# Performance work log

Measured on AMD Instinct MI355X. Metric: run time of the kernel, lower is better.

The kernel has to match this reference:

```python
import jax, jax.numpy as jnp
import numpy as np

T, B, D, H = 512, 512, 512, 512

def setup_inputs() -> dict:
    key = jax.random.key(0)
    k_in, k_wih, k_whh, k_bih, k_bhh = jax.random.split(key, 5)
    s = 1.0 / np.sqrt(H)  # torch RNNCell init scale
    return {
        "inputs": jax.random.normal(k_in, (T, B, D), dtype=jnp.float32),
        "W_ih": jax.random.uniform(k_wih, (H, D), jnp.float32, -s, s),
        "W_hh": jax.random.uniform(k_whh, (H, H), jnp.float32, -s, s),
        "b_ih": jax.random.uniform(k_bih, (H,), jnp.float32, -s, s),
        "b_hh": jax.random.uniform(k_bhh, (H,), jnp.float32, -s, s),
        "hidden_size": H,
    }

def reference(inputs, W_ih, W_hh, b_ih, b_hh, hidden_size):
    # h_{t+1} = tanh(x_t @ W_ih^T + b_ih + h_t @ W_hh^T + b_hh)
    # Original inits hidden with inputs.shape[0] rows (quirk: requires T == B).
    h0 = jnp.zeros((inputs.shape[0], hidden_size), dtype=inputs.dtype)
    # Precompute the input projection for all steps in one big GEMM;
    # the recurrence itself must remain sequential.
    xp = jnp.einsum("tbd,hd->tbh", inputs, W_ih) + b_ih + b_hh  # [T, B, H]

    def step(h, xp_t):
        h = jnp.tanh(xp_t + h @ W_hh.T)
        return h, None

    h_final, _ = jax.lax.scan(step, h0, xp)
    return h_final
```

## Files before the change

### kernel.cpp

```cpp
#include <hip/hip_runtime.h>
#include <stdint.h>

#define TSTEPS 512
#define NB 512
#define ND 512
#define NH 512
#define SENT 0xFFFFFFFFFFFFFFFFull

typedef _Float16 half8 __attribute__((ext_vector_type(8)));
typedef float float4v __attribute__((ext_vector_type(4)));
typedef unsigned long long u64;

__device__ __forceinline__ float fast_tanh(float x) {
  float e = __expf(2.0f * x);
  return 1.0f - 2.0f * __builtin_amdgcn_rcpf(e + 1.0f);
}

#define AL(p)    __hip_atomic_load((p), __ATOMIC_RELAXED, __HIP_MEMORY_SCOPE_AGENT)
#define AS(p, v) __hip_atomic_store((p), (v), __ATOMIC_RELAXED, __HIP_MEMORY_SCOPE_AGENT)

#define LDSBAR()                                                               \
  do {                                                                         \
    asm volatile("s_waitcnt lgkmcnt(0)" ::: "memory");                         \
    __builtin_amdgcn_s_barrier();                                              \
  } while (0)

#define PREFETCH_X(XP, TN)                                                     \
  do {                                                                         \
    const float* xrow_ = x + ((size_t)(TN) * NB + myrow) * ND + kbase + quad * 8; \
    _Pragma("unroll")                                                          \
    for (int kk = 0; kk < 4; ++kk) {                                           \
      XP[kk][0] = *(const float4v*)(xrow_ + kk * 32);                          \
      XP[kk][1] = *(const float4v*)(xrow_ + kk * 32 + 4);                      \
    }                                                                          \
  } while (0)

__global__ void __launch_bounds__(256, 1)
rnn_persistent(const float* __restrict__ x,
               const float* __restrict__ Wih,
               const float* __restrict__ Whh,
               const float* __restrict__ bih,
               const float* __restrict__ bhh,
               float* __restrict__ out,
               _Float16* __restrict__ hbuf)
{
  __shared__ __attribute__((aligned(16))) float red[2][4][16][68];

  const int bid  = blockIdx.x;
  const int grp  = bid & 31;
  const int cwg  = bid >> 5;
  const int wave = threadIdx.x >> 6;
  const int lane = threadIdx.x & 63;
  const int m    = lane & 15;
  const int quad = lane >> 4;
  const int tid  = threadIdx.x;

  const int R     = grp * 16;
  const int C0    = cwg * 64;
  const int kbase = wave * 128;

  half8 wih_f[4][4];
  half8 whh_f[4][4];
  #pragma unroll
  for (int tile = 0; tile < 4; ++tile) {
    const int n = C0 + tile * 16 + m;
    const float* wr_ih = Wih + (size_t)n * ND;
    const float* wr_hh = Whh + (size_t)n * NH;
    #pragma unroll
    for (int kk = 0; kk < 4; ++kk) {
      const int k0 = kbase + kk * 32 + quad * 8;
      half8 a, b;
      #pragma unroll
      for (int j = 0; j < 8; ++j) {
        a[j] = (_Float16)wr_ih[k0 + j];
        b[j] = (_Float16)wr_hh[k0 + j];
      }
      wih_f[kk][tile] = a;
      whh_f[kk][tile] = b;
    }
  }

  const int prow = tid >> 4;
  const int pcol = (tid & 15) * 4;
  float4v bias4;
  #pragma unroll
  for (int j = 0; j < 4; ++j)
    bias4[j] = bih[C0 + pcol + j] + bhh[C0 + pcol + j];

  const int myrow = R + m;
  const int orow  = quad * 4;

  float4v xvA[4][2], xvB[4][2];
  {
    const float* xrow0 = x + (size_t)myrow * ND + kbase + quad * 8;
    #pragma unroll
    for (int kk = 0; kk < 4; ++kk) {
      xvA[kk][0] = *(const float4v*)(xrow0 + kk * 32);
      xvA[kk][1] = *(const float4v*)(xrow0 + kk * 32 + 4);
    }
  }

#define STEP(T, PAR, XU, XP)                                                   \
  {                                                                            \
    const int t_ = (T);                                                        \
        \
    if (t_ >= 2) {                                                             \
      u64* cl = (u64*)(hbuf + (size_t)((t_ + 2) & 3) * NB * NH +               \
                       (size_t)(R + prow) * NH + C0 + pcol);                   \
      AS(cl, SENT);                                                            \
    }                                                                          \
    float4v acc[4];                                                            \
    _Pragma("unroll")                                                          \
    for (int tile = 0; tile < 4; ++tile) acc[tile] = (float4v){0.f,0.f,0.f,0.f};\
                                         \
    _Pragma("unroll")                                                          \
    for (int kk = 0; kk < 4; ++kk) {                                           \
      half8 a;                                                                 \
      _Pragma("unroll")                                                        \
      for (int j = 0; j < 4; ++j) {                                            \
        a[j]     = (_Float16)XU[kk][0][j];                                     \
        a[j + 4] = (_Float16)XU[kk][1][j];                                     \
      }                                                                        \
      _Pragma("unroll")                                                        \
      for (int tile = 0; tile < 4; ++tile)                                     \
        acc[tile] = __builtin_amdgcn_mfma_f32_16x16x32_f16(a, wih_f[kk][tile], acc[tile], 0, 0, 0); \
    }                                                                          \
    if (t_ > 0) {                                                              \
      const int tn_ = (t_ + 1 < TSTEPS) ? (t_ + 1) : t_;                       \
      const _Float16* hb = hbuf + (size_t)(t_ & 3) * NB * NH;                  \
      const u64* hrow = (const u64*)(hb + (size_t)myrow * NH + kbase + quad * 8); \
                                           \
      u64 w0 = AL(hrow + 0), w1 = AL(hrow + 1);                                \
      u64 w2 = AL(hrow + 8), w3 = AL(hrow + 9);                                \
      u64 w4 = AL(hrow + 16), w5 = AL(hrow + 17);                              \
      u64 w6 = AL(hrow + 24), w7 = AL(hrow + 25);                              \
      PREFETCH_X(XP, tn_);                                                     \
      for (;;) {                                                               \
        bool ok = (w0 != SENT) & (w1 != SENT) & (w2 != SENT) & (w3 != SENT) &  \
                  (w4 != SENT) & (w5 != SENT) & (w6 != SENT) & (w7 != SENT);   \
        if (__all((int)ok)) break;                                             \
        __builtin_amdgcn_s_sleep(1);           \
        w0 = AL(hrow + 0); w1 = AL(hrow + 1);                                  \
        w2 = AL(hrow + 8); w3 = AL(hrow + 9);                                  \
        w4 = AL(hrow + 16); w5 = AL(hrow + 17);                                \
        w6 = AL(hrow + 24); w7 = AL(hrow + 25);                                \
      }                                                                        \
      union { u64 u[2]; half8 h; } cvv;                                        \
      cvv.u[0] = w0; cvv.u[1] = w1;                                            \
      _Pragma("unroll")                                                        \
      for (int tile = 0; tile < 4; ++tile)                                     \
        acc[tile] = __builtin_amdgcn_mfma_f32_16x16x32_f16(cvv.h, whh_f[0][tile], acc[tile], 0, 0, 0); \
      cvv.u[0] = w2; cvv.u[1] = w3;                                            \
      _Pragma("unroll")                                                        \
      for (int tile = 0; tile < 4; ++tile)                                     \
        acc[tile] = __builtin_amdgcn_mfma_f32_16x16x32_f16(cvv.h, whh_f[1][tile], acc[tile], 0, 0, 0); \
      cvv.u[0] = w4; cvv.u[1] = w5;                                            \
      _Pragma("unroll")                                                        \
      for (int tile = 0; tile < 4; ++tile)                                     \
        acc[tile] = __builtin_amdgcn_mfma_f32_16x16x32_f16(cvv.h, whh_f[2][tile], acc[tile], 0, 0, 0); \
      cvv.u[0] = w6; cvv.u[1] = w7;                                            \
      _Pragma("unroll")                                                        \
      for (int tile = 0; tile < 4; ++tile)                                     \
        acc[tile] = __builtin_amdgcn_mfma_f32_16x16x32_f16(cvv.h, whh_f[3][tile], acc[tile], 0, 0, 0); \
    } else {                                                                   \
      PREFETCH_X(XP, 1);                                                       \
    }                                                                          \
                       \
    _Pragma("unroll")                                                          \
    for (int tile = 0; tile < 4; ++tile) {                                     \
      _Pragma("unroll")                                                        \
      for (int r = 0; r < 4; ++r)                                              \
        red[PAR][wave][orow + r][tile * 16 + m] = acc[tile][r];                \
    }                                                                          \
    LDSBAR();    \
    float4v s = bias4;                                                         \
    _Pragma("unroll")                                                          \
    for (int w = 0; w < 4; ++w) {                                              \
      const float4v vv = *(const float4v*)&red[PAR][w][prow][pcol];            \
      s[0] += vv[0]; s[1] += vv[1]; s[2] += vv[2]; s[3] += vv[3];              \
    }                                                                          \
    float4v o;                                                                 \
    _Pragma("unroll")                                                          \
    for (int j = 0; j < 4; ++j) o[j] = fast_tanh(s[j]);                        \
    if (t_ < TSTEPS - 1) {                                                     \
      u64* dst = (u64*)(hbuf + (size_t)((t_ + 1) & 3) * NB * NH +              \
                        (size_t)(R + prow) * NH + C0 + pcol);                  \
      union { _Float16 h[4]; u64 u; } pk;                                      \
      _Pragma("unroll")                                                        \
      for (int j = 0; j < 4; ++j) pk.h[j] = (_Float16)o[j];                    \
                                                \
      asm volatile("s_waitcnt vmcnt(0)" ::: "memory");                         \
      AS(dst, pk.u);                                                           \
    } else {                                                                   \
      *(float4v*)(out + (size_t)(R + prow) * NH + C0 + pcol) = o;              \
    }                                                                          \
  }

  for (int t = 0; t < TSTEPS; t += 2) {
    STEP(t,     0, xvA, xvB);
    STEP(t + 1, 1, xvB, xvA);
  }
#undef STEP
}

extern "C" void kernel_launch(void* const* d_in, const int* in_sizes, int n_in,
                              void* d_out, int out_size, void* d_ws, size_t ws_size,
                              hipStream_t stream) {
  const float* x   = (const float*)d_in[0];
  const float* Wih = (const float*)d_in[1];
  const float* Whh = (const float*)d_in[2];
  const float* bih = (const float*)d_in[3];
  const float* bhh = (const float*)d_in[4];
  float* out = (float*)d_out;

  _Float16* hbuf = (_Float16*)d_ws;

  (void)hipMemsetAsync(hbuf, 0xFF, (size_t)4 * NB * NH * sizeof(_Float16), stream);

  rnn_persistent<<<dim3(256), dim3(256), 0, stream>>>(
      x, Wih, Whh, bih, bhh, out, hbuf);
}
```

Measured before the change: 2.149 ms.

## Split recurrent matmul per wave over full K and pipeline input projection one step ahead

Each wave now owns 16 output columns and runs the full K=512 recurrent product itself, which removes the cross-wave LDS reduction and barrier from the critical h-dependency path. The input projection for step t+1 is computed during step t, reduced through LDS before the h wait, and carried in a register. Each lane now loads and spin-checks 32 words of h instead of 8 per step. This raises global traffic and register pressure in the polling loop, and the x prefetch distance grows to two steps.

```diff
diff --git a/kernel.cpp b/kernel.cpp
--- a/kernel.cpp
+++ b/kernel.cpp
@@ -23,16 +23,6 @@
   do {                                                                         \
     asm volatile("s_waitcnt lgkmcnt(0)" ::: "memory");                         \
     __builtin_amdgcn_s_barrier();                                              \
-  } while (0)
-
-#define PREFETCH_X(XP, TN)                                                     \
-  do {                                                                         \
-    const float* xrow_ = x + ((size_t)(TN) * NB + myrow) * ND + kbase + quad * 8; \
-    _Pragma("unroll")                                                          \
-    for (int kk = 0; kk < 4; ++kk) {                                           \
-      XP[kk][0] = *(const float4v*)(xrow_ + kk * 32);                          \
-      XP[kk][1] = *(const float4v*)(xrow_ + kk * 32 + 4);                      \
-    }                                                                          \
   } while (0)
 
 __global__ void __launch_bounds__(256, 1)
@@ -53,50 +43,85 @@
   const int lane = threadIdx.x & 63;
   const int m    = lane & 15;
   const int quad = lane >> 4;
-  const int tid  = threadIdx.x;
 
   const int R     = grp * 16;
   const int C0    = cwg * 64;
   const int kbase = wave * 128;
+  const int myrow = R + m;
 
   half8 wih_f[4][4];
-  half8 whh_f[4][4];
   #pragma unroll
   for (int tile = 0; tile < 4; ++tile) {
-    const int n = C0 + tile * 16 + m;
-    const float* wr_ih = Wih + (size_t)n * ND;
-    const float* wr_hh = Whh + (size_t)n * NH;
+    const float* wr = Wih + (size_t)(C0 + tile * 16 + m) * ND;
     #pragma unroll
     for (int kk = 0; kk < 4; ++kk) {
       const int k0 = kbase + kk * 32 + quad * 8;
-      half8 a, b;
-      #pragma unroll
-      for (int j = 0; j < 8; ++j) {
-        a[j] = (_Float16)wr_ih[k0 + j];
-        b[j] = (_Float16)wr_hh[k0 + j];
-      }
+      half8 a;
+      #pragma unroll
+      for (int j = 0; j < 8; ++j) a[j] = (_Float16)wr[k0 + j];
       wih_f[kk][tile] = a;
-      whh_f[kk][tile] = b;
-    }
-  }
-
-  const int prow = tid >> 4;
-  const int pcol = (tid & 15) * 4;
+    }
+  }
+
+  half8 whh_f[16];
+  {
+    const float* wr = Whh + (size_t)(C0 + wave * 16 + m) * NH;
+    #pragma unroll
+    for (int kk = 0; kk < 16; ++kk) {
+      const int k0 = kk * 32 + quad * 8;
+      half8 a;
+      #pragma unroll
+      for (int j = 0; j < 8; ++j) a[j] = (_Float16)wr[k0 + j];
+      whh_f[kk] = a;
+    }
+  }
+
+  const int pubcol = C0 + wave * 16 + quad * 4;
   float4v bias4;
   #pragma unroll
   for (int j = 0; j < 4; ++j)
-    bias4[j] = bih[C0 + pcol + j] + bhh[C0 + pcol + j];
-
-  const int myrow = R + m;
-  const int orow  = quad * 4;
+    bias4[j] = bih[pubcol + j] + bhh[pubcol + j];
 
   float4v xvA[4][2], xvB[4][2];
+  float4v xp_cur;
   {
-    const float* xrow0 = x + (size_t)myrow * ND + kbase + quad * 8;
-    #pragma unroll
-    for (int kk = 0; kk < 4; ++kk) {
-      xvA[kk][0] = *(const float4v*)(xrow0 + kk * 32);
-      xvA[kk][1] = *(const float4v*)(xrow0 + kk * 32 + 4);
+    const float* xr = x + (size_t)myrow * ND + kbase + quad * 8;
+    float4v x0[4][2];
+    #pragma unroll
+    for (int kk = 0; kk < 4; ++kk) {
+      x0[kk][0] = *(const float4v*)(xr + kk * 32);
+      x0[kk][1] = *(const float4v*)(xr + kk * 32 + 4);
+    }
+    float4v xacc[4];
+    #pragma unroll
+    for (int tile = 0; tile < 4; ++tile) xacc[tile] = (float4v){0.f,0.f,0.f,0.f};
+    #pragma unroll
+    for (int kk = 0; kk < 4; ++kk) {
+      half8 a;
+      #pragma unroll
+      for (int j = 0; j < 4; ++j) {
+        a[j] = (_Float16)x0[kk][0][j];
+        a[j + 4] = (_Float16)x0[kk][1][j];
+      }
+      #pragma unroll
+      for (int tile = 0; tile < 4; ++tile)
+        xacc[tile] = __builtin_amdgcn_mfma_f32_16x16x32_f16(wih_f[kk][tile], a, xacc[tile], 0, 0, 0);
+    }
+    #pragma unroll
+    for (int tile = 0; tile < 4; ++tile)
+      *(float4v*)&red[0][wave][m][tile * 16 + quad * 4] = xacc[tile];
+    LDSBAR();
+    xp_cur = bias4;
+    #pragma unroll
+    for (int w = 0; w < 4; ++w) {
+      const float4v v = *(const float4v*)&red[0][w][m][wave * 16 + quad * 4];
+      xp_cur[0] += v[0]; xp_cur[1] += v[1]; xp_cur[2] += v[2]; xp_cur[3] += v[3];
+    }
+    const float* xr1 = x + ((size_t)1 * NB + myrow) * ND + kbase + quad * 8;
+    #pragma unroll
+    for (int kk = 0; kk < 4; ++kk) {
+      xvA[kk][0] = *(const float4v*)(xr1 + kk * 32);
+      xvA[kk][1] = *(const float4v*)(xr1 + kk * 32 + 4);
     }
   }
 
@@ -105,100 +130,105 @@
     const int t_ = (T);                                                        \
         \
     if (t_ >= 2) {                                                             \
-      u64* cl = (u64*)(hbuf + (size_t)((t_ + 2) & 3) * NB * NH +               \
-                       (size_t)(R + prow) * NH + C0 + pcol);                   \
-      AS(cl, SENT);                                                            \
-    }                                                                          \
-    float4v acc[4];                                                            \
-    _Pragma("unroll")                                                          \
-    for (int tile = 0; tile < 4; ++tile) acc[tile] = (float4v){0.f,0.f,0.f,0.f};\
-                                         \
+      AS((u64*)(hbuf + (size_t)((t_ + 2) & 3) * NB * NH +                      \
+                (size_t)myrow * NH + pubcol), SENT);                           \
+    }                                                                          \
+                        \
+    const u64* hbase = (const u64*)(hbuf + (size_t)(t_ & 3) * NB * NH +        \
+                                    (size_t)myrow * NH);                       \
+    u64 hw[32];                                                                \
+    if (t_ > 0) {                                                              \
+      _Pragma("unroll")                                                        \
+      for (int i = 0; i < 32; ++i)                                             \
+        hw[i] = AL(hbase + (i >> 1) * 8 + quad * 2 + (i & 1));                 \
+    }                                                                          \
+           \
+    {                                                                          \
+      const int tn_ = (t_ + 2 < TSTEPS) ? (t_ + 2) : (TSTEPS - 1);             \
+      const float* xr_ = x + ((size_t)tn_ * NB + myrow) * ND + kbase + quad * 8; \
+      _Pragma("unroll")                                                        \
+      for (int kk = 0; kk < 4; ++kk) {                                         \
+        XP[kk][0] = *(const float4v*)(xr_ + kk * 32);                          \
+        XP[kk][1] = *(const float4v*)(xr_ + kk * 32 + 4);                      \
+      }                                                                        \
+    }                                                                          \
+    __builtin_amdgcn_sched_barrier(0);  \
+      \
+    float4v xacc[4];                                                           \
+    _Pragma("unroll")                                                          \
+    for (int tile = 0; tile < 4; ++tile) xacc[tile] = (float4v){0.f,0.f,0.f,0.f};\
     _Pragma("unroll")                                                          \
     for (int kk = 0; kk < 4; ++kk) {                                           \
       half8 a;                                                                 \
       _Pragma("unroll")                                                        \
       for (int j = 0; j < 4; ++j) {                                            \
-        a[j]     = (_Float16)XU[kk][0][j];                                     \
+        a[j] = (_Float16)XU[kk][0][j];                                         \
         a[j + 4] = (_Float16)XU[kk][1][j];                                     \
       }                                                                        \
       _Pragma("unroll")                                                        \
       for (int tile = 0; tile < 4; ++tile)                                     \
-        acc[tile] = __builtin_amdgcn_mfma_f32_16x16x32_f16(a, wih_f[kk][tile], acc[tile], 0, 0, 0); \
-    }                                                                          \
+        xacc[tile] = __builtin_amdgcn_mfma_f32_16x16x32_f16(wih_f[kk][tile], a, xacc[tile], 0, 0, 0); \
+    }                                                                          \
+    _Pragma("unroll")                                                          \
+    for (int tile = 0; tile < 4; ++tile)                                       \
+      *(float4v*)&red[PAR][wave][m][tile * 16 + quad * 4] = xacc[tile];        \
+    LDSBAR();                \
+    float4v xp_next = bias4;                                                   \
+    _Pragma("unroll")                                                          \
+    for (int w = 0; w < 4; ++w) {                                              \
+      const float4v v = *(const float4v*)&red[PAR][w][m][wave * 16 + quad * 4];\
+      xp_next[0] += v[0]; xp_next[1] += v[1];                                  \
+      xp_next[2] += v[2]; xp_next[3] += v[3];                                  \
+    }                                                                          \
+               \
+    float4v hacc[4];                                                           \
+    _Pragma("unroll")                                                          \
+    for (int c = 0; c < 4; ++c) hacc[c] = (float4v){0.f,0.f,0.f,0.f};          \
     if (t_ > 0) {                                                              \
-      const int tn_ = (t_ + 1 < TSTEPS) ? (t_ + 1) : t_;                       \
-      const _Float16* hb = hbuf + (size_t)(t_ & 3) * NB * NH;                  \
-      const u64* hrow = (const u64*)(hb + (size_t)myrow * NH + kbase + quad * 8); \
-                                           \
-      u64 w0 = AL(hrow + 0), w1 = AL(hrow + 1);                                \
-      u64 w2 = AL(hrow + 8), w3 = AL(hrow + 9);                                \
-      u64 w4 = AL(hrow + 16), w5 = AL(hrow + 17);                              \
-      u64 w6 = AL(hrow + 24), w7 = AL(hrow + 25);                              \
-      PREFETCH_X(XP, tn_);                                                     \
       for (;;) {                                                               \
-        bool ok = (w0 != SENT) & (w1 != SENT) & (w2 != SENT) & (w3 != SENT) &  \
-                  (w4 != SENT) & (w5 != SENT) & (w6 != SENT) & (w7 != SENT);   \
+        bool ok = true;                                                        \
+        _Pragma("unroll")                                                      \
+        for (int i = 0; i < 32; ++i) ok &= (hw[i] != SENT);                    \
         if (__all((int)ok)) break;                                             \
-        __builtin_amdgcn_s_sleep(1);           \
-        w0 = AL(hrow + 0); w1 = AL(hrow + 1);                                  \
-        w2 = AL(hrow + 8); w3 = AL(hrow + 9);                                  \
-        w4 = AL(hrow + 16); w5 = AL(hrow + 17);                                \
-        w6 = AL(hrow + 24); w7 = AL(hrow + 25);                                \
-      }                                                                        \
-      union { u64 u[2]; half8 h; } cvv;                                        \
-      cvv.u[0] = w0; cvv.u[1] = w1;                                            \
-      _Pragma("unroll")                                                        \
-      for (int tile = 0; tile < 4; ++tile)                                     \
-        acc[tile] = __builtin_amdgcn_mfma_f32_16x16x32_f16(cvv.h, whh_f[0][tile], acc[tile], 0, 0, 0); \
-      cvv.u[0] = w2; cvv.u[1] = w3;                                            \
-      _Pragma("unroll")                                                        \
-      for (int tile = 0; tile < 4; ++tile)                                     \
-        acc[tile] = __builtin_amdgcn_mfma_f32_16x16x32_f16(cvv.h, whh_f[1][tile], acc[tile], 0, 0, 0); \
-      cvv.u[0] = w4; cvv.u[1] = w5;                                            \
-      _Pragma("unroll")                                                        \
-      for (int tile = 0; tile < 4; ++tile)                                     \
-        acc[tile] = __builtin_amdgcn_mfma_f32_16x16x32_f16(cvv.h, whh_f[2][tile], acc[tile], 0, 0, 0); \
-      cvv.u[0] = w6; cvv.u[1] = w7;                                            \
-      _Pragma("unroll")                                                        \
-      for (int tile = 0; tile < 4; ++tile)                                     \
-        acc[tile] = __builtin_amdgcn_mfma_f32_16x16x32_f16(cvv.h, whh_f[3][tile], acc[tile], 0, 0, 0); \
-    } else {                                                                   \
-      PREFETCH_X(XP, 1);                                                       \
-    }                                                                          \
-                       \
-    _Pragma("unroll")                                                          \
-    for (int tile = 0; tile < 4; ++tile) {                                     \
-      _Pragma("unroll")                                                        \
-      for (int r = 0; r < 4; ++r)                                              \
-        red[PAR][wave][orow + r][tile * 16 + m] = acc[tile][r];                \
-    }                                                                          \
-    LDSBAR();    \
-    float4v s = bias4;                                                         \
-    _Pragma("unroll")                                                          \
-    for (int w = 0; w < 4; ++w) {                                              \
-      const float4v vv = *(const float4v*)&red[PAR][w][prow][pcol];            \
-      s[0] += vv[0]; s[1] += vv[1]; s[2] += vv[2]; s[3] += vv[3];              \
+        __builtin_amdgcn_s_sleep(1);                                           \
+        _Pragma("unroll")                                                      \
+        for (int i = 0; i < 32; ++i)                                           \
+          hw[i] = AL(hbase + (i >> 1) * 8 + quad * 2 + (i & 1));               \
+      }                                                                        \
+      _Pragma("unroll")                                                        \
+      for (int kk = 0; kk < 16; ++kk) {                                        \
+        union { u64 u[2]; half8 h; } cv;                                       \
+        cv.u[0] = hw[2 * kk]; cv.u[1] = hw[2 * kk + 1];                        \
+        hacc[kk & 3] = __builtin_amdgcn_mfma_f32_16x16x32_f16(whh_f[kk], cv.h, hacc[kk & 3], 0, 0, 0); \
+      }                                                                        \
+    }                                                                          \
+    float4v s = xp_cur;                                                        \
+    _Pragma("unroll")                                                          \
+    for (int c = 0; c < 4; ++c) {                                              \
+      s[0] += hacc[c][0]; s[1] += hacc[c][1];                                  \
+      s[2] += hacc[c][2]; s[3] += hacc[c][3];                                  \
     }                                                                          \
     float4v o;                                                                 \
     _Pragma("unroll")                                                          \
     for (int j = 0; j < 4; ++j) o[j] = fast_tanh(s[j]);                        \
     if (t_ < TSTEPS - 1) {                                                     \
       u64* dst = (u64*)(hbuf + (size_t)((t_ + 1) & 3) * NB * NH +              \
-                        (size_t)(R + prow) * NH + C0 + pcol);                  \
+                        (size_t)myrow * NH + pubcol);                          \
       union { _Float16 h[4]; u64 u; } pk;                                      \
       _Pragma("unroll")                                                        \
       for (int j = 0; j < 4; ++j) pk.h[j] = (_Float16)o[j];                    \
-                                                \
+         \
       asm volatile("s_waitcnt vmcnt(0)" ::: "memory");                         \
       AS(dst, pk.u);                                                           \
     } else {                                                                   \
-      *(float4v*)(out + (size_t)(R + prow) * NH + C0 + pcol) = o;              \
-    }                                                                          \
+      *(float4v*)(out + (size_t)myrow * NH + pubcol) = o;                      \
+    }                                                                          \
+    xp_cur = xp_next;                                                          \
   }
 
   for (int t = 0; t < TSTEPS; t += 2) {
-    STEP(t,     0, xvA, xvB);
-    STEP(t + 1, 1, xvB, xvA);
+    STEP(t,     1, xvA, xvB);
+    STEP(t + 1, 0, xvB, xvA);
   }
 #undef STEP
 }
```

Measured after the change: 5.845 ms. 172% more time.
